# Kernel tuning notes

Hardware: AMD Instinct MI355X
Metric: run time of the kernel (lower is better)

The kernel has to match this reference:

```python
import jax, jax.numpy as jnp
import numpy as np

B, S, D = 4, 2048, 1024
E, TOP_K = 8, 2
N_FF = 4096
H = int(2 * N_FF / 3)  # 2730, Expert hidden when ffn_multiplier is None


def setup_inputs() -> dict:
    key = jax.random.key(0)
    ks = jax.random.split(key, 8)
    s = 0.02
    return {
        "x": jax.random.normal(ks[0], (B, S, D), jnp.float32),
        "noise": jax.random.normal(ks[1], (B, S, E), jnp.float32),
        "w_route": jax.random.normal(ks[2], (D, E), jnp.float32) * s,
        "b_route": jnp.zeros((E,), jnp.float32),
        "w_noise": jax.random.normal(ks[3], (D, E), jnp.float32) * s,
        "b_noise": jnp.zeros((E,), jnp.float32),
        "w_proj": jax.random.normal(ks[4], (E, D, 2 * H), jnp.float32) * s,  # SwiGLU proj per expert
        "w_down": jax.random.normal(ks[5], (E, H, D), jnp.float32) * s,
    }


def reference(x, noise, w_route, b_route, w_noise, b_noise, w_proj, w_down):
    b, s, d = x.shape
    e = w_route.shape[1]
    n = b * s
    capacity = int(n * TOP_K / e * 1.0)  # capacity_factor = 1.0

    # --- NoisyTopkRouter (temperature = 1.0) ---
    logits = jnp.einsum("bsd,de->bse", x, w_route) + b_route
    noise_scale = jax.nn.softplus(jnp.einsum("bsd,de->bse", x, w_noise) + b_noise)
    noisy = logits + noise * noise_scale
    top_v, top_i = jax.lax.top_k(noisy, TOP_K)  # [b,s,k]
    # softmax over -inf-filled sparse logits == softmax over the top-k values,
    # scattered back to the expert axis
    probs_k = jax.nn.softmax(top_v, axis=-1)  # [b,s,k]
    routing = jnp.sum(jax.nn.one_hot(top_i, e, dtype=x.dtype) * probs_k[..., None], axis=-2)  # [b,s,e]
    router_prob = routing.mean(axis=(0, 1))
    aux_loss = jnp.sum((router_prob - 1.0 / e) ** 2)

    # --- dispatch ---
    flat_x = x.reshape(n, d)
    flat_gate = routing.reshape(n, e)
    hit = jnp.any(top_i.reshape(n, TOP_K)[:, :, None] == jnp.arange(e)[None, None, :], axis=1)  # [n,e]

    def per_expert(mask_e, gate_e, wp, wd):
        # keep first `capacity` selected tokens, in token order (matches torch nonzero order)
        keep = mask_e & (jnp.cumsum(mask_e) <= capacity)
        sel = jnp.argsort(~keep, stable=True)[:capacity]  # selected token ids first, in order
        valid = keep[sel].astype(flat_x.dtype)
        xin = flat_x[sel]  # [capacity, d]
        x1, x2 = jnp.split(xin @ wp, 2, axis=-1)
        out = (jax.nn.silu(x1) * x2) @ wd  # [capacity, d]
        w = gate_e[sel] * valid
        return sel, out * w[:, None]

    sel, contrib = jax.vmap(per_expert)(hit.T, flat_gate.T, w_proj, w_down)  # [e,cap], [e,cap,d]
    updates = jnp.zeros_like(flat_x).at[sel.reshape(-1)].add(contrib.reshape(-1, d))
    return updates.reshape(b, s, d), aux_loss
```

## Files before the change

### kernel.cpp

```cpp
#include <hip/hip_runtime.h>
#include <cstdint>
#include <cstddef>

#define NTOK 8192
#define DMODEL 1024
#define NEXP 8
#define CAP 2048
#define HFF 2730
#define HFF2 5460
#define KPAD 2752

typedef float f32x4 __attribute__((ext_vector_type(4)));
typedef __attribute__((ext_vector_type(8))) short short8;

__device__ inline unsigned short f2bf(float f) {
  union { float f; unsigned u; } v; v.f = f;
  unsigned u = v.u;
  return (unsigned short)((u + 0x7FFFu + ((u >> 16) & 1u)) >> 16);
}
__device__ inline float bf2f(unsigned short s) {
  union { unsigned u; float f; } v; v.u = ((unsigned)s) << 16; return v.f;
}

typedef __attribute__((address_space(1))) const void g_void;
typedef __attribute__((address_space(3))) void l_void;
__device__ __forceinline__ void dma16(const void* g, void* l) {
  __builtin_amdgcn_global_load_lds((g_void*)g, (l_void*)l, 16, 0, 0);
}

__global__ void cast_x_kernel(const float* __restrict__ x, unsigned short* __restrict__ xb) {
  size_t i = ((size_t)blockIdx.x * 256 + threadIdx.x) * 8;
  float4 v0 = *(const float4*)(x + i);
  float4 v1 = *(const float4*)(x + i + 4);
  union { short8 v; unsigned short s[8]; } p;
  p.s[0] = f2bf(v0.x); p.s[1] = f2bf(v0.y); p.s[2] = f2bf(v0.z); p.s[3] = f2bf(v0.w);
  p.s[4] = f2bf(v1.x); p.s[5] = f2bf(v1.y); p.s[6] = f2bf(v1.z); p.s[7] = f2bf(v1.w);
  *(short8*)(xb + i) = p.v;
}

__global__ void router_kernel(const float* __restrict__ x,
                              const float* __restrict__ noise,
                              const float* __restrict__ w_route,
                              const float* __restrict__ b_route,
                              const float* __restrict__ w_noise,
                              const float* __restrict__ b_noise,
                              int* __restrict__ topi,
                              float* __restrict__ gates) {
  const int lane = threadIdx.x & 63;
  const int wave = threadIdx.x >> 6;
  const int tok = blockIdx.x * 4 + wave;
  const float* xr = x + (size_t)tok * DMODEL;

  double aR[8], aN[8];
#pragma unroll
  for (int e = 0; e < 8; e++) { aR[e] = 0.0; aN[e] = 0.0; }

  for (int d = lane; d < DMODEL; d += 64) {
    double xv = (double)xr[d];
    const float* wr = w_route + d * 8;
    const float* wn = w_noise + d * 8;
#pragma unroll
    for (int e = 0; e < 8; e++) {
      aR[e] += xv * (double)wr[e];
      aN[e] += xv * (double)wn[e];
    }
  }
#pragma unroll
  for (int off = 32; off > 0; off >>= 1) {
#pragma unroll
    for (int e = 0; e < 8; e++) {
      aR[e] += __shfl_down(aR[e], (unsigned)off, 64);
      aN[e] += __shfl_down(aN[e], (unsigned)off, 64);
    }
  }
  if (lane == 0) {
    double nv[8];
#pragma unroll
    for (int e = 0; e < 8; e++) {
      double lg = aR[e] + (double)b_route[e];
      double ns = aN[e] + (double)b_noise[e];
      double sp = fmax(ns, 0.0) + log1p(exp(-fabs(ns)));
      nv[e] = lg + (double)noise[(size_t)tok * 8 + e] * sp;
    }
    int i0 = 0;
#pragma unroll
    for (int e = 1; e < 8; e++) if (nv[e] > nv[i0]) i0 = e;
    int i1 = (i0 == 0) ? 1 : 0;
#pragma unroll
    for (int e = 0; e < 8; e++) if (e != i0 && nv[e] > nv[i1]) i1 = e;
    double r = exp(nv[i1] - nv[i0]);
    float g0 = (float)(1.0 / (1.0 + r));
    float g1 = (float)(r / (1.0 + r));
    topi[tok * 2] = i0; topi[tok * 2 + 1] = i1;
    gates[tok * 2] = g0; gates[tok * 2 + 1] = g1;
  }
}

__global__ void aux_kernel(const int* __restrict__ topi,
                           const float* __restrict__ gates,
                           float* __restrict__ out) {
  const int t = threadIdx.x;
  float s[8];
#pragma unroll
  for (int e = 0; e < 8; e++) s[e] = 0.f;
  for (int i = t; i < NTOK; i += 256) {
    int i0 = topi[2 * i], i1 = topi[2 * i + 1];
    float g0 = gates[2 * i], g1 = gates[2 * i + 1];
#pragma unroll
    for (int e = 0; e < 8; e++)
      s[e] += (i0 == e ? g0 : 0.f) + (i1 == e ? g1 : 0.f);
  }
  __shared__ float sh[256][8];
#pragma unroll
  for (int e = 0; e < 8; e++) sh[t][e] = s[e];
  __syncthreads();
  for (int stride = 128; stride > 0; stride >>= 1) {
    if (t < stride) {
#pragma unroll
      for (int e = 0; e < 8; e++) sh[t][e] += sh[t + stride][e];
    }
    __syncthreads();
  }
  if (t == 0) {
    float aux = 0.f;
#pragma unroll
    for (int e = 0; e < 8; e++) {
      float p = sh[0][e] / (float)NTOK - 0.125f;
      aux += p * p;
    }
    out[(size_t)NTOK * DMODEL] = aux;
  }
}

__global__ void dispatch_kernel(const int* __restrict__ topi,
                                const float* __restrict__ gates,
                                int* __restrict__ sel,
                                float* __restrict__ gsel,
                                int* __restrict__ slot) {
  const int e = blockIdx.x;
  const int t = threadIdx.x;
  const int lane = t & 63;
  const int w = t >> 6;
  __shared__ int waveCnt[16];
  __shared__ int runningS;
  if (t == 0) runningS = 0;
  __syncthreads();

  for (int base = 0; base < NTOK; base += 1024) {
    int tok = base + t;
    int i0 = topi[2 * tok], i1 = topi[2 * tok + 1];
    bool hit = (i0 == e) || (i1 == e);
    int kth = (i0 == e) ? 0 : 1;
    float g = gates[2 * tok + kth];
    unsigned long long m = __ballot(hit);
    int prefix = __popcll(m & ((1ull << lane) - 1ull));
    if (lane == 63) waveCnt[w] = prefix + (hit ? 1 : 0);
    __syncthreads();
    int off = runningS;
    for (int ww = 0; ww < w; ww++) off += waveCnt[ww];
    int pos = off + prefix;
    if (hit) {
      if (pos < CAP) {
        sel[e * CAP + pos] = tok; gsel[e * CAP + pos] = g;
        slot[2 * tok + kth] = pos;
      } else {
        slot[2 * tok + kth] = -1;
      }
    }
    __syncthreads();
    if (t == 0) {
      int sacc = 0;
#pragma unroll
      for (int ww = 0; ww < 16; ww++) sacc += waveCnt[ww];
      runningS += sacc;
    }
    __syncthreads();
  }
  for (int p = runningS + t; p < CAP; p += 1024) { sel[e * CAP + p] = 0; gsel[e * CAP + p] = 0.f; }
}

__global__ void transpose_wp_kernel(const float* __restrict__ wp,
                                    unsigned short* __restrict__ wpT) {
  const int e = blockIdx.z, d0 = blockIdx.y * 32, f0 = blockIdx.x * 32;
  __shared__ unsigned short tile[32][33];
  const int t = threadIdx.x;
  {
    int ld = t >> 3, lf4 = (t & 7) * 4;
    if (f0 + lf4 < HFF2) {
      float4 v = *(const float4*)(wp + (size_t)e * DMODEL * HFF2 + (size_t)(d0 + ld) * HFF2 + f0 + lf4);
      tile[ld][lf4 + 0] = f2bf(v.x);
      tile[ld][lf4 + 1] = f2bf(v.y);
      tile[ld][lf4 + 2] = f2bf(v.z);
      tile[ld][lf4 + 3] = f2bf(v.w);
    }
  }
  __syncthreads();
  {
    int lf = t >> 3, ldq = (t & 7) * 4;
    if (f0 + lf < HFF2) {
      ushort4 o = make_ushort4(tile[ldq + 0][lf], tile[ldq + 1][lf],
                               tile[ldq + 2][lf], tile[ldq + 3][lf]);
      *(ushort4*)(wpT + (size_t)e * HFF2 * DMODEL + (size_t)(f0 + lf) * DMODEL + d0 + ldq) = o;
    }
  }
}

__global__ void transpose_wd_kernel(const float* __restrict__ wd,
                                    unsigned short* __restrict__ wdT) {
  const int e = blockIdx.z, d0 = blockIdx.y * 32, k0 = blockIdx.x * 32;
  __shared__ unsigned short tile[32][33];
  const int t = threadIdx.x;
  {
    int lk = t >> 3, ld4 = (t & 7) * 4;
    int k = k0 + lk;
    if (k < HFF) {
      float4 v = *(const float4*)(wd + (size_t)e * HFF * DMODEL + (size_t)k * DMODEL + d0 + ld4);
      tile[lk][ld4 + 0] = f2bf(v.x);
      tile[lk][ld4 + 1] = f2bf(v.y);
      tile[lk][ld4 + 2] = f2bf(v.z);
      tile[lk][ld4 + 3] = f2bf(v.w);
    } else {
      tile[lk][ld4 + 0] = 0; tile[lk][ld4 + 1] = 0;
      tile[lk][ld4 + 2] = 0; tile[lk][ld4 + 3] = 0;
    }
  }
  __syncthreads();
  {
    int ld = t >> 3, lkq = (t & 7) * 4;
    ushort4 o = make_ushort4(tile[lkq + 0][ld], tile[lkq + 1][ld],
                             tile[lkq + 2][ld], tile[lkq + 3][ld]);
    *(ushort4*)(wdT + (size_t)e * DMODEL * KPAD + (size_t)(d0 + ld) * KPAD + k0 + lkq) = o;
  }
}

__global__ __launch_bounds__(512, 2)
void gemm1_kernel(const unsigned short* __restrict__ xb,
                  const unsigned short* __restrict__ wpT,
                  const int* __restrict__ sel,
                  unsigned short* __restrict__ h) {
  const int e = blockIdx.z;
  const int m0 = blockIdx.x * 256;
  const int n0 = blockIdx.y * 128;

  __shared__ __align__(16) unsigned short smem[4 * 16384];

  const int t = threadIdx.x;
  const int lane = t & 63;
  const int w = t >> 6;
  const int wr = w >> 2;
  const int wc = w & 3;
  const int fr = lane & 15;
  const int fq = lane >> 4;
  const int csw = (fq ^ ((fr >> 1) & 3)) * 8;

  const int r0 = t >> 2;
  const int sw = ((t & 3) ^ ((t >> 3) & 3)) * 8;
  const int tok0 = sel[e * CAP + m0 + r0];
  const int tok1 = sel[e * CAP + m0 + 128 + r0];
  const unsigned short* ga0 = xb + (size_t)tok0 * DMODEL + sw;
  const unsigned short* ga1 = xb + (size_t)tok1 * DMODEL + sw;
  const size_t ebase = (size_t)e * HFF2;
  int c0 = n0 + r0; if (c0 >= HFF) c0 = HFF - 1;
  const unsigned short* gb1 = wpT + (ebase + (size_t)c0) * DMODEL + sw;
  const unsigned short* gb2 = wpT + (ebase + (size_t)(HFF + c0)) * DMODEL + sw;

  const int dOff = w * 1024;

  f32x4 acc1[8][2], acc2[8][2];
#pragma unroll
  for (int i = 0; i < 8; i++)
#pragma unroll
    for (int j = 0; j < 2; j++) { acc1[i][j] = (f32x4)0.f; acc2[i][j] = (f32x4)0.f; }

  auto stageA = [&](int kt) {
    char* b = (char*)smem + (size_t)(kt & 3) * 32768;
    const int k0 = kt * 32;
    dma16(ga0 + k0, b + dOff);
    dma16(ga1 + k0, b + 8192 + dOff);
  };
  auto stageB = [&](int kt) {
    char* b = (char*)smem + (size_t)(kt & 3) * 32768;
    const int k0 = kt * 32;
    dma16(gb1 + k0, b + 16384 + dOff);
    dma16(gb2 + k0, b + 24576 + dOff);
  };

  stageA(0); stageB(0); stageA(1); stageB(1); stageA(2); stageB(2);

  for (int kt = 0; kt < 32; ++kt) {
    if (kt < 30)       asm volatile("s_waitcnt vmcnt(8)" ::: "memory");
    else if (kt == 30) asm volatile("s_waitcnt vmcnt(4)" ::: "memory");
    else               asm volatile("s_waitcnt vmcnt(0)" ::: "memory");
    __builtin_amdgcn_s_barrier();
    asm volatile("" ::: "memory");

    const unsigned short* Ab  = smem + (kt & 3) * 16384;
    const unsigned short* B1b = Ab + 8192;
    const unsigned short* B2b = Ab + 12288;

    short8 a[8], b1[2], b2[2];
#pragma unroll
    for (int i = 0; i < 8; i++)
      a[i] = *(const short8*)(Ab + (wr * 128 + i * 16 + fr) * 32 + csw);
#pragma unroll
    for (int j = 0; j < 2; j++)
      b1[j] = *(const short8*)(B1b + (wc * 32 + j * 16 + fr) * 32 + csw);
    if (kt < 29) stageA(kt + 3);
    __builtin_amdgcn_s_setprio(1);
#pragma unroll
    for (int i = 0; i < 8; i++)
#pragma unroll
      for (int j = 0; j < 2; j++)
        acc1[i][j] = __builtin_amdgcn_mfma_f32_16x16x32_bf16(a[i], b1[j], acc1[i][j], 0, 0, 0);
    __builtin_amdgcn_s_setprio(0);
#pragma unroll
    for (int j = 0; j < 2; j++)
      b2[j] = *(const short8*)(B2b + (wc * 32 + j * 16 + fr) * 32 + csw);
    if (kt < 29) stageB(kt + 3);
    __builtin_amdgcn_s_setprio(1);
#pragma unroll
    for (int i = 0; i < 8; i++)
#pragma unroll
      for (int j = 0; j < 2; j++)
        acc2[i][j] = __builtin_amdgcn_mfma_f32_16x16x32_bf16(a[i], b2[j], acc2[i][j], 0, 0, 0);
    __builtin_amdgcn_s_setprio(0);
  }

#pragma unroll
  for (int i = 0; i < 8; i++) {
#pragma unroll
    for (int j = 0; j < 2; j++) {
      const int col = n0 + wc * 32 + j * 16 + fr;
      if (col < KPAD) {
#pragma unroll
        for (int r = 0; r < 4; r++) {
          const int row = m0 + wr * 128 + i * 16 + fq * 4 + r;
          float v1 = acc1[i][j][r], v2 = acc2[i][j][r];
          float hv = (col < HFF) ? (v1 / (1.f + __expf(-v1))) * v2 : 0.f;
          h[((size_t)e * CAP + row) * KPAD + col] = f2bf(hv);
        }
      }
    }
  }
}

__global__ __launch_bounds__(512, 2)
void gemm2_kernel(const unsigned short* __restrict__ h,
                  const unsigned short* __restrict__ wdT,
                  unsigned short* __restrict__ contrib) {
  const int e = blockIdx.z;
  const int m0 = blockIdx.x * 256;
  const int n0 = blockIdx.y * 256;

  __shared__ __align__(16) unsigned short smem[4 * 16384];

  const int t = threadIdx.x;
  const int lane = t & 63;
  const int w = t >> 6;
  const int wr = w >> 2;
  const int wc = w & 3;
  const int fr = lane & 15;
  const int fq = lane >> 4;
  const int csw = (fq ^ ((fr >> 1) & 3)) * 8;

  const int r0 = t >> 2;
  const int sw = ((t & 3) ^ ((t >> 3) & 3)) * 8;
  const unsigned short* ga0 = h + ((size_t)e * CAP + m0 + r0) * KPAD + sw;
  const unsigned short* ga1 = h + ((size_t)e * CAP + m0 + 128 + r0) * KPAD + sw;
  const unsigned short* gb0 = wdT + ((size_t)e * DMODEL + n0 + r0) * KPAD + sw;
  const unsigned short* gb1 = wdT + ((size_t)e * DMODEL + n0 + 128 + r0) * KPAD + sw;

  const int dOff = w * 1024;

  f32x4 acc[8][4];
#pragma unroll
  for (int i = 0; i < 8; i++)
#pragma unroll
    for (int j = 0; j < 4; j++) acc[i][j] = (f32x4)0.f;

  auto stageA = [&](int kt) {
    char* b = (char*)smem + (size_t)(kt & 3) * 32768;
    const int k0 = kt * 32;
    dma16(ga0 + k0, b + dOff);
    dma16(ga1 + k0, b + 8192 + dOff);
  };
  auto stageB = [&](int kt) {
    char* b = (char*)smem + (size_t)(kt & 3) * 32768;
    const int k0 = kt * 32;
    dma16(gb0 + k0, b + 16384 + dOff);
    dma16(gb1 + k0, b + 24576 + dOff);
  };

  stageA(0); stageB(0); stageA(1); stageB(1); stageA(2); stageB(2);

  for (int kt = 0; kt < 86; ++kt) {
    if (kt < 84)       asm volatile("s_waitcnt vmcnt(8)" ::: "memory");
    else if (kt == 84) asm volatile("s_waitcnt vmcnt(4)" ::: "memory");
    else               asm volatile("s_waitcnt vmcnt(0)" ::: "memory");
    __builtin_amdgcn_s_barrier();
    asm volatile("" ::: "memory");

    const unsigned short* Ab = smem + (kt & 3) * 16384;
    const unsigned short* Bb = Ab + 8192;

    short8 a[8], b[4];
#pragma unroll
    for (int i = 0; i < 8; i++)
      a[i] = *(const short8*)(Ab + (wr * 128 + i * 16 + fr) * 32 + csw);
#pragma unroll
    for (int j = 0; j < 4; j++)
      b[j] = *(const short8*)(Bb + (wc * 64 + j * 16 + fr) * 32 + csw);
    if (kt < 83) { stageA(kt + 3); stageB(kt + 3); }
    __builtin_amdgcn_s_setprio(1);
#pragma unroll
    for (int i = 0; i < 8; i++)
#pragma unroll
      for (int j = 0; j < 4; j++)
        acc[i][j] = __builtin_amdgcn_mfma_f32_16x16x32_bf16(a[i], b[j], acc[i][j], 0, 0, 0);
    __builtin_amdgcn_s_setprio(0);
  }

#pragma unroll
  for (int i = 0; i < 8; i++) {
#pragma unroll
    for (int j = 0; j < 4; j++) {
      const int col = n0 + wc * 64 + j * 16 + fr;
#pragma unroll
      for (int r = 0; r < 4; r++) {
        const int row = m0 + wr * 128 + i * 16 + fq * 4 + r;
        contrib[((size_t)e * CAP + row) * DMODEL + col] = f2bf(acc[i][j][r]);
      }
    }
  }
}

__global__ void combine_kernel(const unsigned short* __restrict__ contrib,
                               const int* __restrict__ topi,
                               const int* __restrict__ slot,
                               const float* __restrict__ gates,
                               float* __restrict__ out) {
  const int tok = blockIdx.x;
  const int t = threadIdx.x;
  const int e0 = topi[2 * tok], e1 = topi[2 * tok + 1];
  const int s0 = slot[2 * tok], s1 = slot[2 * tok + 1];
  const float g0 = gates[2 * tok], g1 = gates[2 * tok + 1];
  float4 acc = make_float4(0.f, 0.f, 0.f, 0.f);
  if (s0 >= 0) {
    ushort4 c = *(const ushort4*)(contrib + ((size_t)(e0 * CAP + s0)) * DMODEL + t * 4);
    acc.x += g0 * bf2f(c.x); acc.y += g0 * bf2f(c.y);
    acc.z += g0 * bf2f(c.z); acc.w += g0 * bf2f(c.w);
  }
  if (s1 >= 0) {
    ushort4 c = *(const ushort4*)(contrib + ((size_t)(e1 * CAP + s1)) * DMODEL + t * 4);
    acc.x += g1 * bf2f(c.x); acc.y += g1 * bf2f(c.y);
    acc.z += g1 * bf2f(c.z); acc.w += g1 * bf2f(c.w);
  }
  *(float4*)(out + (size_t)tok * DMODEL + t * 4) = acc;
}

extern "C" void kernel_launch(void* const* d_in, const int* in_sizes, int n_in,
                              void* d_out, int out_size, void* d_ws, size_t ws_size,
                              hipStream_t stream) {
  const float* x = (const float*)d_in[0];
  const float* noise = (const float*)d_in[1];
  const float* w_route = (const float*)d_in[2];
  const float* b_route = (const float*)d_in[3];
  const float* w_noise = (const float*)d_in[4];
  const float* b_noise = (const float*)d_in[5];
  const float* w_proj = (const float*)d_in[6];
  const float* w_down = (const float*)d_in[7];
  float* out = (float*)d_out;

  char* ws = (char*)d_ws;
  const size_t WT_BYTES = (size_t)NEXP * HFF2 * DMODEL * 2;
  const size_t WDT_BYTES = (size_t)NEXP * DMODEL * KPAD * 2;
  const size_t H_BYTES = (size_t)NEXP * CAP * KPAD * 2;
  unsigned short* wT = (unsigned short*)ws;
  unsigned short* contrib = (unsigned short*)(ws + WDT_BYTES);
  unsigned short* hbuf = (unsigned short*)(ws + WT_BYTES);
  char* p = ws + WT_BYTES + H_BYTES;
  int* sel = (int*)p;          p += (size_t)NEXP * CAP * 4;
  float* gsel = (float*)p;     p += (size_t)NEXP * CAP * 4;
  int* topi = (int*)p;         p += (size_t)NTOK * 2 * 4;
  float* gates = (float*)p;    p += (size_t)NTOK * 2 * 4;
  int* slot = (int*)p;

  unsigned short* xb = (unsigned short*)d_out;

  hipLaunchKernelGGL(cast_x_kernel, dim3(NTOK * DMODEL / (256 * 8)), dim3(256), 0, stream, x, xb);
  hipLaunchKernelGGL(router_kernel, dim3(NTOK / 4), dim3(256), 0, stream,
                     x, noise, w_route, b_route, w_noise, b_noise, topi, gates);
  hipLaunchKernelGGL(dispatch_kernel, dim3(NEXP), dim3(1024), 0, stream, topi, gates, sel, gsel, slot);
  hipLaunchKernelGGL(transpose_wp_kernel, dim3(171, 32, NEXP), dim3(256), 0, stream, w_proj, wT);
  hipLaunchKernelGGL(gemm1_kernel, dim3(CAP / 256, 22, NEXP), dim3(512), 0, stream, xb, wT, sel, hbuf);
  hipLaunchKernelGGL(transpose_wd_kernel, dim3(KPAD / 32, DMODEL / 32, NEXP), dim3(256), 0, stream, w_down, wT);
  hipLaunchKernelGGL(gemm2_kernel, dim3(CAP / 256, DMODEL / 256, NEXP), dim3(512), 0, stream,
                     hbuf, wT, contrib);
  hipLaunchKernelGGL(combine_kernel, dim3(NTOK), dim3(256), 0, stream,
                     contrib, topi, slot, gates, out);
  hipLaunchKernelGGL(aux_kernel, dim3(1), dim3(256), 0, stream, topi, gates, out);
}
```

Before: 791.5 us.

## Split GEMM main loops into two ping-pong phases with explicit barriers and sched fences

Restructures the k-loop of both expert GEMM kernels into two half-phases. Each phase loads half of the A fragments plus the B fragments from LDS, issues one staging DMA, synchronises with an extra s_barrier and lgkmcnt wait, then runs an MFMA cluster fenced by sched_barrier. This is meant to interleave LDS reads, global DMA and MFMA work across waves in a ping-pong schedule and to cut register pressure by holding 4 A fragments instead of 8. The cost is four extra workgroup barriers per iteration, which may stall if the waves do not overlap as intended.

```diff
diff --git a/kernel.cpp b/kernel.cpp
--- a/kernel.cpp
+++ b/kernel.cpp
@@ -27,6 +27,7 @@
 __device__ __forceinline__ void dma16(const void* g, void* l) {
   __builtin_amdgcn_global_load_lds((g_void*)g, (l_void*)l, 16, 0, 0);
 }
+__device__ __forceinline__ void keep(short8 v) { asm volatile("" :: "v"(v)); }
 
 __global__ void cast_x_kernel(const float* __restrict__ x, unsigned short* __restrict__ xb) {
   size_t i = ((size_t)blockIdx.x * 256 + threadIdx.x) * 8;
@@ -298,32 +299,54 @@
     const unsigned short* B1b = Ab + 8192;
     const unsigned short* B2b = Ab + 12288;
 
-    short8 a[8], b1[2], b2[2];
-#pragma unroll
-    for (int i = 0; i < 8; i++)
+    short8 a[4], b1[2], b2[2];
+#pragma unroll
+    for (int i = 0; i < 4; i++) {
       a[i] = *(const short8*)(Ab + (wr * 128 + i * 16 + fr) * 32 + csw);
-#pragma unroll
-    for (int j = 0; j < 2; j++)
+      keep(a[i]);
+    }
+#pragma unroll
+    for (int j = 0; j < 2; j++) {
       b1[j] = *(const short8*)(B1b + (wc * 32 + j * 16 + fr) * 32 + csw);
+      b2[j] = *(const short8*)(B2b + (wc * 32 + j * 16 + fr) * 32 + csw);
+      keep(b1[j]); keep(b2[j]);
+    }
     if (kt < 29) stageA(kt + 3);
+    __builtin_amdgcn_s_barrier();
+    asm volatile("s_waitcnt lgkmcnt(0)" ::: "memory");
+    __builtin_amdgcn_sched_barrier(0);
     __builtin_amdgcn_s_setprio(1);
 #pragma unroll
-    for (int i = 0; i < 8; i++)
-#pragma unroll
-      for (int j = 0; j < 2; j++)
+    for (int i = 0; i < 4; i++)
+#pragma unroll
+      for (int j = 0; j < 2; j++) {
         acc1[i][j] = __builtin_amdgcn_mfma_f32_16x16x32_bf16(a[i], b1[j], acc1[i][j], 0, 0, 0);
+        acc2[i][j] = __builtin_amdgcn_mfma_f32_16x16x32_bf16(a[i], b2[j], acc2[i][j], 0, 0, 0);
+      }
     __builtin_amdgcn_s_setprio(0);
-#pragma unroll
-    for (int j = 0; j < 2; j++)
-      b2[j] = *(const short8*)(B2b + (wc * 32 + j * 16 + fr) * 32 + csw);
+    __builtin_amdgcn_sched_barrier(0);
+    __builtin_amdgcn_s_barrier();
+
+    short8 a2[4];
+#pragma unroll
+    for (int i = 0; i < 4; i++) {
+      a2[i] = *(const short8*)(Ab + (wr * 128 + (i + 4) * 16 + fr) * 32 + csw);
+      keep(a2[i]);
+    }
     if (kt < 29) stageB(kt + 3);
+    __builtin_amdgcn_s_barrier();
+    asm volatile("s_waitcnt lgkmcnt(0)" ::: "memory");
+    __builtin_amdgcn_sched_barrier(0);
     __builtin_amdgcn_s_setprio(1);
 #pragma unroll
-    for (int i = 0; i < 8; i++)
-#pragma unroll
-      for (int j = 0; j < 2; j++)
-        acc2[i][j] = __builtin_amdgcn_mfma_f32_16x16x32_bf16(a[i], b2[j], acc2[i][j], 0, 0, 0);
+    for (int i = 0; i < 4; i++)
+#pragma unroll
+      for (int j = 0; j < 2; j++) {
+        acc1[i + 4][j] = __builtin_amdgcn_mfma_f32_16x16x32_bf16(a2[i], b1[j], acc1[i + 4][j], 0, 0, 0);
+        acc2[i + 4][j] = __builtin_amdgcn_mfma_f32_16x16x32_bf16(a2[i], b2[j], acc2[i + 4][j], 0, 0, 0);
+      }
     __builtin_amdgcn_s_setprio(0);
+    __builtin_amdgcn_sched_barrier(0);
   }
 
 #pragma unroll
@@ -403,21 +426,49 @@
     const unsigned short* Ab = smem + (kt & 3) * 16384;
     const unsigned short* Bb = Ab + 8192;
 
-    short8 a[8], b[4];
-#pragma unroll
-    for (int i = 0; i < 8; i++)
+    short8 a[4], b[4];
+#pragma unroll
+    for (int i = 0; i < 4; i++) {
       a[i] = *(const short8*)(Ab + (wr * 128 + i * 16 + fr) * 32 + csw);
-#pragma unroll
-    for (int j = 0; j < 4; j++)
+      keep(a[i]);
+    }
+#pragma unroll
+    for (int j = 0; j < 4; j++) {
       b[j] = *(const short8*)(Bb + (wc * 64 + j * 16 + fr) * 32 + csw);
-    if (kt < 83) { stageA(kt + 3); stageB(kt + 3); }
+      keep(b[j]);
+    }
+    if (kt < 83) stageA(kt + 3);
+    __builtin_amdgcn_s_barrier();
+    asm volatile("s_waitcnt lgkmcnt(0)" ::: "memory");
+    __builtin_amdgcn_sched_barrier(0);
     __builtin_amdgcn_s_setprio(1);
 #pragma unroll
-    for (int i = 0; i < 8; i++)
+    for (int i = 0; i < 4; i++)
 #pragma unroll
       for (int j = 0; j < 4; j++)
         acc[i][j] = __builtin_amdgcn_mfma_f32_16x16x32_bf16(a[i], b[j], acc[i][j], 0, 0, 0);
     __builtin_amdgcn_s_setprio(0);
+    __builtin_amdgcn_sched_barrier(0);
+    __builtin_amdgcn_s_barrier();
+
+    short8 a2[4];
+#pragma unroll
+    for (int i = 0; i < 4; i++) {
+      a2[i] = *(const short8*)(Ab + (wr * 128 + (i + 4) * 16 + fr) * 32 + csw);
+      keep(a2[i]);
+    }
+    if (kt < 83) stageB(kt + 3);
+    __builtin_amdgcn_s_barrier();
+    asm volatile("s_waitcnt lgkmcnt(0)" ::: "memory");
+    __builtin_amdgcn_sched_barrier(0);
+    __builtin_amdgcn_s_setprio(1);
+#pragma unroll
+    for (int i = 0; i < 4; i++)
+#pragma unroll
+      for (int j = 0; j < 4; j++)
+        acc[i + 4][j] = __builtin_amdgcn_mfma_f32_16x16x32_bf16(a2[i], b[j], acc[i + 4][j], 0, 0, 0);
+    __builtin_amdgcn_s_setprio(0);
+    __builtin_amdgcn_sched_barrier(0);
   }
 
 #pragma unroll
```

Result: slower. 836.4 us (+5.7%).

## Load GEMM A operands directly into registers and remap block order for locality

Applied to the files above, without the earlier changes.

Both expert GEMMs now load the A operand (gathered token rows, or the hidden activations) straight from global memory into registers. Loads for the next K step are double-buffered in registers, so only the weight tiles go through LDS, which halves shared memory per block. The wait counts are adjusted to match the new load pattern. Block indices are also remapped so that neighbouring blocks share an expert and M tile, aiming at better L2 reuse. The trade-off is that each of the four column waves re-fetches the same A rows, and the per-lane 16-byte row-strided global loads coalesce less well than the old LDS staging.

```diff
diff --git a/kernel.cpp b/kernel.cpp
--- a/kernel.cpp
+++ b/kernel.cpp
@@ -238,11 +238,14 @@
                   const unsigned short* __restrict__ wpT,
                   const int* __restrict__ sel,
                   unsigned short* __restrict__ h) {
-  const int e = blockIdx.z;
-  const int m0 = blockIdx.x * 256;
-  const int n0 = blockIdx.y * 128;
-
-  __shared__ __align__(16) unsigned short smem[4 * 16384];
+  const int L = blockIdx.x + 8 * (blockIdx.y + 22 * blockIdx.z);
+  const int rr = L & 7, q = L >> 3;
+  const int G = (q % 22) * 8 + rr;
+  const int e = G / 22;
+  const int n0 = (G % 22) * 128;
+  const int m0 = (q / 22) * 256;
+
+  __shared__ __align__(16) unsigned short smem[4 * 8192];
 
   const int t = threadIdx.x;
   const int lane = t & 63;
@@ -255,16 +258,18 @@
 
   const int r0 = t >> 2;
   const int sw = ((t & 3) ^ ((t >> 3) & 3)) * 8;
-  const int tok0 = sel[e * CAP + m0 + r0];
-  const int tok1 = sel[e * CAP + m0 + 128 + r0];
-  const unsigned short* ga0 = xb + (size_t)tok0 * DMODEL + sw;
-  const unsigned short* ga1 = xb + (size_t)tok1 * DMODEL + sw;
   const size_t ebase = (size_t)e * HFF2;
   int c0 = n0 + r0; if (c0 >= HFF) c0 = HFF - 1;
   const unsigned short* gb1 = wpT + (ebase + (size_t)c0) * DMODEL + sw;
   const unsigned short* gb2 = wpT + (ebase + (size_t)(HFF + c0)) * DMODEL + sw;
-
-  const int dOff = w * 1024;
+  const int dOffB = w * 1024;
+
+  const unsigned short* pa[8];
+#pragma unroll
+  for (int i = 0; i < 8; i++) {
+    int tok = sel[e * CAP + m0 + wr * 128 + i * 16 + fr];
+    pa[i] = xb + (size_t)tok * DMODEL + fq * 8;
+  }
 
   f32x4 acc1[8][2], acc2[8][2];
 #pragma unroll
@@ -272,59 +277,51 @@
 #pragma unroll
     for (int j = 0; j < 2; j++) { acc1[i][j] = (f32x4)0.f; acc2[i][j] = (f32x4)0.f; }
 
-  auto stageA = [&](int kt) {
-    char* b = (char*)smem + (size_t)(kt & 3) * 32768;
+  auto stageB = [&](int kt) {
+    char* b = (char*)smem + (size_t)(kt & 3) * 16384;
     const int k0 = kt * 32;
-    dma16(ga0 + k0, b + dOff);
-    dma16(ga1 + k0, b + 8192 + dOff);
+    dma16(gb1 + k0, b + dOffB);
+    dma16(gb2 + k0, b + 8192 + dOffB);
   };
-  auto stageB = [&](int kt) {
-    char* b = (char*)smem + (size_t)(kt & 3) * 32768;
-    const int k0 = kt * 32;
-    dma16(gb1 + k0, b + 16384 + dOff);
-    dma16(gb2 + k0, b + 24576 + dOff);
-  };
-
-  stageA(0); stageB(0); stageA(1); stageB(1); stageA(2); stageB(2);
-
-  for (int kt = 0; kt < 32; ++kt) {
-    if (kt < 30)       asm volatile("s_waitcnt vmcnt(8)" ::: "memory");
-    else if (kt == 30) asm volatile("s_waitcnt vmcnt(4)" ::: "memory");
-    else               asm volatile("s_waitcnt vmcnt(0)" ::: "memory");
+
+  short8 aA[8], aB[8];
+#pragma unroll
+  for (int i = 0; i < 8; i++) aA[i] = *(const short8*)(pa[i]);
+  stageB(0); stageB(1); stageB(2);
+
+  auto step = [&](int kt, short8 (&ac)[8], short8 (&an)[8]) {
+    if (kt == 0)      asm volatile("s_waitcnt vmcnt(4)" ::: "memory");
+    else if (kt < 30) asm volatile("s_waitcnt vmcnt(2)" ::: "memory");
+    else              asm volatile("s_waitcnt vmcnt(0)" ::: "memory");
     __builtin_amdgcn_s_barrier();
     asm volatile("" ::: "memory");
 
-    const unsigned short* Ab  = smem + (kt & 3) * 16384;
-    const unsigned short* B1b = Ab + 8192;
-    const unsigned short* B2b = Ab + 12288;
-
-    short8 a[8], b1[2], b2[2];
-#pragma unroll
-    for (int i = 0; i < 8; i++)
-      a[i] = *(const short8*)(Ab + (wr * 128 + i * 16 + fr) * 32 + csw);
-#pragma unroll
-    for (int j = 0; j < 2; j++)
+    const unsigned short* B1b = smem + (size_t)(kt & 3) * 8192;
+    const unsigned short* B2b = B1b + 4096;
+    short8 b1[2], b2[2];
+#pragma unroll
+    for (int j = 0; j < 2; j++) {
       b1[j] = *(const short8*)(B1b + (wc * 32 + j * 16 + fr) * 32 + csw);
-    if (kt < 29) stageA(kt + 3);
-    __builtin_amdgcn_s_setprio(1);
-#pragma unroll
-    for (int i = 0; i < 8; i++)
-#pragma unroll
-      for (int j = 0; j < 2; j++)
-        acc1[i][j] = __builtin_amdgcn_mfma_f32_16x16x32_bf16(a[i], b1[j], acc1[i][j], 0, 0, 0);
-    __builtin_amdgcn_s_setprio(0);
-#pragma unroll
-    for (int j = 0; j < 2; j++)
       b2[j] = *(const short8*)(B2b + (wc * 32 + j * 16 + fr) * 32 + csw);
+    }
+    if (kt < 31) {
+      const int k1 = (kt + 1) * 32;
+#pragma unroll
+      for (int i = 0; i < 8; i++) an[i] = *(const short8*)(pa[i] + k1);
+    }
     if (kt < 29) stageB(kt + 3);
     __builtin_amdgcn_s_setprio(1);
 #pragma unroll
     for (int i = 0; i < 8; i++)
 #pragma unroll
-      for (int j = 0; j < 2; j++)
-        acc2[i][j] = __builtin_amdgcn_mfma_f32_16x16x32_bf16(a[i], b2[j], acc2[i][j], 0, 0, 0);
+      for (int j = 0; j < 2; j++) {
+        acc1[i][j] = __builtin_amdgcn_mfma_f32_16x16x32_bf16(ac[i], b1[j], acc1[i][j], 0, 0, 0);
+        acc2[i][j] = __builtin_amdgcn_mfma_f32_16x16x32_bf16(ac[i], b2[j], acc2[i][j], 0, 0, 0);
+      }
     __builtin_amdgcn_s_setprio(0);
-  }
+  };
+
+  for (int kt = 0; kt < 32; kt += 2) { step(kt, aA, aB); step(kt + 1, aB, aA); }
 
 #pragma unroll
   for (int i = 0; i < 8; i++) {
@@ -348,11 +345,14 @@
 void gemm2_kernel(const unsigned short* __restrict__ h,
                   const unsigned short* __restrict__ wdT,
                   unsigned short* __restrict__ contrib) {
-  const int e = blockIdx.z;
-  const int m0 = blockIdx.x * 256;
-  const int n0 = blockIdx.y * 256;
-
-  __shared__ __align__(16) unsigned short smem[4 * 16384];
+  const int L = blockIdx.x + 8 * (blockIdx.y + 4 * blockIdx.z);
+  const int rr = L & 7, q = L >> 3;
+  const int G = (q % 4) * 8 + rr;
+  const int e = G / 4;
+  const int n0 = (G % 4) * 256;
+  const int m0 = (q / 4) * 256;
+
+  __shared__ __align__(16) unsigned short smem[4 * 8192];
 
   const int t = threadIdx.x;
   const int lane = t & 63;
@@ -365,12 +365,14 @@
 
   const int r0 = t >> 2;
   const int sw = ((t & 3) ^ ((t >> 3) & 3)) * 8;
-  const unsigned short* ga0 = h + ((size_t)e * CAP + m0 + r0) * KPAD + sw;
-  const unsigned short* ga1 = h + ((size_t)e * CAP + m0 + 128 + r0) * KPAD + sw;
   const unsigned short* gb0 = wdT + ((size_t)e * DMODEL + n0 + r0) * KPAD + sw;
   const unsigned short* gb1 = wdT + ((size_t)e * DMODEL + n0 + 128 + r0) * KPAD + sw;
-
-  const int dOff = w * 1024;
+  const int dOffB = w * 1024;
+
+  const unsigned short* pa[8];
+#pragma unroll
+  for (int i = 0; i < 8; i++)
+    pa[i] = h + ((size_t)e * CAP + m0 + wr * 128 + i * 16 + fr) * KPAD + fq * 8;
 
   f32x4 acc[8][4];
 #pragma unroll
@@ -378,47 +380,46 @@
 #pragma unroll
     for (int j = 0; j < 4; j++) acc[i][j] = (f32x4)0.f;
 
-  auto stageA = [&](int kt) {
-    char* b = (char*)smem + (size_t)(kt & 3) * 32768;
+  auto stageB = [&](int kt) {
+    char* b = (char*)smem + (size_t)(kt & 3) * 16384;
     const int k0 = kt * 32;
-    dma16(ga0 + k0, b + dOff);
-    dma16(ga1 + k0, b + 8192 + dOff);
+    dma16(gb0 + k0, b + dOffB);
+    dma16(gb1 + k0, b + 8192 + dOffB);
   };
-  auto stageB = [&](int kt) {
-    char* b = (char*)smem + (size_t)(kt & 3) * 32768;
-    const int k0 = kt * 32;
-    dma16(gb0 + k0, b + 16384 + dOff);
-    dma16(gb1 + k0, b + 24576 + dOff);
-  };
-
-  stageA(0); stageB(0); stageA(1); stageB(1); stageA(2); stageB(2);
-
-  for (int kt = 0; kt < 86; ++kt) {
-    if (kt < 84)       asm volatile("s_waitcnt vmcnt(8)" ::: "memory");
-    else if (kt == 84) asm volatile("s_waitcnt vmcnt(4)" ::: "memory");
-    else               asm volatile("s_waitcnt vmcnt(0)" ::: "memory");
+
+  short8 aA[8], aB[8];
+#pragma unroll
+  for (int i = 0; i < 8; i++) aA[i] = *(const short8*)(pa[i]);
+  stageB(0); stageB(1); stageB(2);
+
+  auto step = [&](int kt, short8 (&ac)[8], short8 (&an)[8]) {
+    if (kt == 0)      asm volatile("s_waitcnt vmcnt(4)" ::: "memory");
+    else if (kt < 84) asm volatile("s_waitcnt vmcnt(2)" ::: "memory");
+    else              asm volatile("s_waitcnt vmcnt(0)" ::: "memory");
     __builtin_amdgcn_s_barrier();
     asm volatile("" ::: "memory");
 
-    const unsigned short* Ab = smem + (kt & 3) * 16384;
-    const unsigned short* Bb = Ab + 8192;
-
-    short8 a[8], b[4];
-#pragma unroll
-    for (int i = 0; i < 8; i++)
-      a[i] = *(const short8*)(Ab + (wr * 128 + i * 16 + fr) * 32 + csw);
+    const unsigned short* Bb = smem + (size_t)(kt & 3) * 8192;
+    short8 b[4];
 #pragma unroll
     for (int j = 0; j < 4; j++)
       b[j] = *(const short8*)(Bb + (wc * 64 + j * 16 + fr) * 32 + csw);
-    if (kt < 83) { stageA(kt + 3); stageB(kt + 3); }
+    if (kt < 85) {
+      const int k1 = (kt + 1) * 32;
+#pragma unroll
+      for (int i = 0; i < 8; i++) an[i] = *(const short8*)(pa[i] + k1);
+    }
+    if (kt < 83) stageB(kt + 3);
     __builtin_amdgcn_s_setprio(1);
 #pragma unroll
     for (int i = 0; i < 8; i++)
 #pragma unroll
       for (int j = 0; j < 4; j++)
-        acc[i][j] = __builtin_amdgcn_mfma_f32_16x16x32_bf16(a[i], b[j], acc[i][j], 0, 0, 0);
+        acc[i][j] = __builtin_amdgcn_mfma_f32_16x16x32_bf16(ac[i], b[j], acc[i][j], 0, 0, 0);
     __builtin_amdgcn_s_setprio(0);
-  }
+  };
+
+  for (int kt = 0; kt < 86; kt += 2) { step(kt, aA, aB); step(kt + 1, aB, aA); }
 
 #pragma unroll
   for (int i = 0; i < 8; i++) {
```

After: 1.242 ms. 56.9% more time.

## Remap GEMM block order for XCD locality, widen wp transpose, hoist B2 loads

Applied to the files above, without the earlier changes.

Both expert GEMMs now remap the linear block index so that blocks dispatched round-robin to the same XCD (L & 7) work on the same expert and neighbouring N tiles. The intent is better L2 reuse of weight and activation tiles within each XCD's private cache. The w_proj transpose uses 64x64 tiles with 16-byte stores instead of 32x32 tiles with 8-byte stores, cutting block count and improving store width. gemm1 also loads the B2 fragments alongside B1 before the first MFMA batch, which raises register pressure in exchange for fewer LDS-wait stalls between the two MFMA groups.

```diff
diff --git a/kernel.cpp b/kernel.cpp
--- a/kernel.cpp
+++ b/kernel.cpp
@@ -181,26 +181,35 @@
 
 __global__ void transpose_wp_kernel(const float* __restrict__ wp,
                                     unsigned short* __restrict__ wpT) {
-  const int e = blockIdx.z, d0 = blockIdx.y * 32, f0 = blockIdx.x * 32;
-  __shared__ unsigned short tile[32][33];
-  const int t = threadIdx.x;
-  {
-    int ld = t >> 3, lf4 = (t & 7) * 4;
-    if (f0 + lf4 < HFF2) {
-      float4 v = *(const float4*)(wp + (size_t)e * DMODEL * HFF2 + (size_t)(d0 + ld) * HFF2 + f0 + lf4);
-      tile[ld][lf4 + 0] = f2bf(v.x);
-      tile[ld][lf4 + 1] = f2bf(v.y);
-      tile[ld][lf4 + 2] = f2bf(v.z);
-      tile[ld][lf4 + 3] = f2bf(v.w);
+  const int e = blockIdx.z, d0 = blockIdx.y * 64, f0 = blockIdx.x * 64;
+  __shared__ unsigned short tile[64][68];
+  const int t = threadIdx.x;
+  const int ld = t >> 4;
+  const int lf4 = (t & 15) * 4;
+#pragma unroll
+  for (int p = 0; p < 4; p++) {
+    int d = d0 + p * 16 + ld;
+    int f = f0 + lf4;
+    if (f < HFF2) {
+      float4 v = *(const float4*)(wp + ((size_t)e * DMODEL + d) * HFF2 + f);
+      tile[lf4 + 0][p * 16 + ld] = f2bf(v.x);
+      tile[lf4 + 1][p * 16 + ld] = f2bf(v.y);
+      tile[lf4 + 2][p * 16 + ld] = f2bf(v.z);
+      tile[lf4 + 3][p * 16 + ld] = f2bf(v.w);
     }
   }
   __syncthreads();
-  {
-    int lf = t >> 3, ldq = (t & 7) * 4;
-    if (f0 + lf < HFF2) {
-      ushort4 o = make_ushort4(tile[ldq + 0][lf], tile[ldq + 1][lf],
-                               tile[ldq + 2][lf], tile[ldq + 3][lf]);
-      *(ushort4*)(wpT + (size_t)e * HFF2 * DMODEL + (size_t)(f0 + lf) * DMODEL + d0 + ldq) = o;
+  const int dq = (t & 7) * 8;
+#pragma unroll
+  for (int q = 0; q < 2; q++) {
+    int fl = q * 32 + (t >> 3);
+    int f = f0 + fl;
+    if (f < HFF2) {
+      ushort4 u0 = *(const ushort4*)&tile[fl][dq];
+      ushort4 u1 = *(const ushort4*)&tile[fl][dq + 4];
+      union { ushort4 u[2]; short8 v; } pk;
+      pk.u[0] = u0; pk.u[1] = u1;
+      *(short8*)(wpT + (size_t)e * HFF2 * DMODEL + (size_t)f * DMODEL + d0 + dq) = pk.v;
     }
   }
 }
@@ -238,9 +247,12 @@
                   const unsigned short* __restrict__ wpT,
                   const int* __restrict__ sel,
                   unsigned short* __restrict__ h) {
-  const int e = blockIdx.z;
-  const int m0 = blockIdx.x * 256;
-  const int n0 = blockIdx.y * 128;
+  const int L = blockIdx.x + 8 * (blockIdx.y + 22 * blockIdx.z);
+  const int r = L & 7, q = L >> 3;
+  const int G = (q % 22) * 8 + r;
+  const int e = G / 22;
+  const int n0 = (G % 22) * 128;
+  const int m0 = (q / 22) * 256;
 
   __shared__ __align__(16) unsigned short smem[4 * 16384];
 
@@ -297,14 +309,15 @@
     const unsigned short* Ab  = smem + (kt & 3) * 16384;
     const unsigned short* B1b = Ab + 8192;
     const unsigned short* B2b = Ab + 12288;
-
     short8 a[8], b1[2], b2[2];
 #pragma unroll
     for (int i = 0; i < 8; i++)
       a[i] = *(const short8*)(Ab + (wr * 128 + i * 16 + fr) * 32 + csw);
 #pragma unroll
-    for (int j = 0; j < 2; j++)
+    for (int j = 0; j < 2; j++) {
       b1[j] = *(const short8*)(B1b + (wc * 32 + j * 16 + fr) * 32 + csw);
+      b2[j] = *(const short8*)(B2b + (wc * 32 + j * 16 + fr) * 32 + csw);
+    }
     if (kt < 29) stageA(kt + 3);
     __builtin_amdgcn_s_setprio(1);
 #pragma unroll
@@ -313,9 +326,6 @@
       for (int j = 0; j < 2; j++)
         acc1[i][j] = __builtin_amdgcn_mfma_f32_16x16x32_bf16(a[i], b1[j], acc1[i][j], 0, 0, 0);
     __builtin_amdgcn_s_setprio(0);
-#pragma unroll
-    for (int j = 0; j < 2; j++)
-      b2[j] = *(const short8*)(B2b + (wc * 32 + j * 16 + fr) * 32 + csw);
     if (kt < 29) stageB(kt + 3);
     __builtin_amdgcn_s_setprio(1);
 #pragma unroll
@@ -333,9 +343,9 @@
       const int col = n0 + wc * 32 + j * 16 + fr;
       if (col < KPAD) {
 #pragma unroll
-        for (int r = 0; r < 4; r++) {
-          const int row = m0 + wr * 128 + i * 16 + fq * 4 + r;
-          float v1 = acc1[i][j][r], v2 = acc2[i][j][r];
+        for (int r2 = 0; r2 < 4; r2++) {
+          const int row = m0 + wr * 128 + i * 16 + fq * 4 + r2;
+          float v1 = acc1[i][j][r2], v2 = acc2[i][j][r2];
           float hv = (col < HFF) ? (v1 / (1.f + __expf(-v1))) * v2 : 0.f;
           h[((size_t)e * CAP + row) * KPAD + col] = f2bf(hv);
         }
@@ -348,9 +358,12 @@
 void gemm2_kernel(const unsigned short* __restrict__ h,
                   const unsigned short* __restrict__ wdT,
                   unsigned short* __restrict__ contrib) {
-  const int e = blockIdx.z;
-  const int m0 = blockIdx.x * 256;
-  const int n0 = blockIdx.y * 256;
+  const int L = blockIdx.x + 8 * (blockIdx.y + 4 * blockIdx.z);
+  const int r = L & 7, q = L >> 3;
+  const int G = (q % 4) * 8 + r;
+  const int e = G / 4;
+  const int n0 = (G % 4) * 256;
+  const int m0 = (q / 4) * 256;
 
   __shared__ __align__(16) unsigned short smem[4 * 16384];
 
@@ -402,7 +415,6 @@
 
     const unsigned short* Ab = smem + (kt & 3) * 16384;
     const unsigned short* Bb = Ab + 8192;
-
     short8 a[8], b[4];
 #pragma unroll
     for (int i = 0; i < 8; i++)
@@ -426,9 +438,9 @@
     for (int j = 0; j < 4; j++) {
       const int col = n0 + wc * 64 + j * 16 + fr;
 #pragma unroll
-      for (int r = 0; r < 4; r++) {
-        const int row = m0 + wr * 128 + i * 16 + fq * 4 + r;
-        contrib[((size_t)e * CAP + row) * DMODEL + col] = f2bf(acc[i][j][r]);
+      for (int r2 = 0; r2 < 4; r2++) {
+        const int row = m0 + wr * 128 + i * 16 + fq * 4 + r2;
+        contrib[((size_t)e * CAP + row) * DMODEL + col] = f2bf(acc[i][j][r2]);
       }
     }
   }
@@ -491,7 +503,7 @@
   hipLaunchKernelGGL(router_kernel, dim3(NTOK / 4), dim3(256), 0, stream,
                      x, noise, w_route, b_route, w_noise, b_noise, topi, gates);
   hipLaunchKernelGGL(dispatch_kernel, dim3(NEXP), dim3(1024), 0, stream, topi, gates, sel, gsel, slot);
-  hipLaunchKernelGGL(transpose_wp_kernel, dim3(171, 32, NEXP), dim3(256), 0, stream, w_proj, wT);
+  hipLaunchKernelGGL(transpose_wp_kernel, dim3(86, 16, NEXP), dim3(256), 0, stream, w_proj, wT);
   hipLaunchKernelGGL(gemm1_kernel, dim3(CAP / 256, 22, NEXP), dim3(512), 0, stream, xb, wT, sel, hbuf);
   hipLaunchKernelGGL(transpose_wd_kernel, dim3(KPAD / 32, DMODEL / 32, NEXP), dim3(256), 0, stream, w_down, wT);
   hipLaunchKernelGGL(gemm2_kernel, dim3(CAP / 256, DMODEL / 256, NEXP), dim3(512), 0, stream,
```

Result: no change. 785.8 us (-0.7%).
